# Kernel tuning notes

Hardware: AMD Instinct MI355X
Metric: run time of the kernel (lower is better)

The kernel has to match this reference:

```python
import jax, jax.numpy as jnp
import numpy as np


def setup_inputs() -> dict:
    key = jax.random.key(0)
    ks = jax.random.split(key, 10)
    b, n, d = 4, 64, 64
    E = 4096
    node_emb = jax.random.normal(ks[0], (b * n, d), dtype=jnp.float32)
    path_emb = jax.random.normal(ks[1], (b, n, n, d), dtype=jnp.float32)
    edge_index = jax.random.randint(ks[2], (2, E), 0, b * n, dtype=jnp.int64)
    # learned params, stored as (in, out) so application is x @ W + b
    W_hz = jax.random.normal(ks[3], (d, d), dtype=jnp.float32) / np.sqrt(d)
    b_hz = jnp.zeros((d,), dtype=jnp.float32)
    W_zz = jax.random.normal(ks[4], (3 * d, d), dtype=jnp.float32) / np.sqrt(3 * d)
    b_zz = jnp.zeros((d,), dtype=jnp.float32)
    W_nm = jax.random.normal(ks[5], (2 * d, d), dtype=jnp.float32) / np.sqrt(2 * d)
    b_nm = jnp.zeros((d,), dtype=jnp.float32)
    return {
        "node_emb": node_emb, "path_emb": path_emb, "edge_index": edge_index,
        "W_hz": W_hz, "b_hz": b_hz, "W_zz": W_zz, "b_zz": b_zz,
        "W_nm": W_nm, "b_nm": b_nm,
    }


def reference(node_emb, path_emb, edge_index, W_hz, b_hz, W_zz, b_zz, W_nm, b_nm):
    b, n, _, d = path_emb.shape
    # ---- PathConv (aggr='max') ----
    z = path_emb @ W_hz + b_hz                                  # (b, n, n, d)
    # tropical (max-plus) matmul over paths: z_conv[b,i,j,d] = max_k z[b,i,k,d] + z[b,k,j,d]
    z_conv = jnp.max(z[:, :, :, None, :] + z[:, None, :, :, :], axis=2)  # (b, n, n, d)
    z = jnp.maximum(z_conv, z)                                  # path_aggr mode='max'
    ne = node_emb.reshape(b, n, d)
    n_i = jnp.broadcast_to(ne[:, :, None, :], (b, n, n, d))
    n_j = jnp.broadcast_to(ne[:, None, :, :], (b, n, n, d))
    u_path = jax.nn.relu(jnp.concatenate([n_i, z, n_j], axis=-1) @ W_zz + b_zz)
    # ---- MPLayer (default message = x_j, aggr='add'; edge_attr unused) ----
    src, dst = edge_index[0], edge_index[1]
    aggr_msg = jax.ops.segment_sum(node_emb[src], dst, num_segments=node_emb.shape[0])
    u_node = jax.nn.relu(jnp.concatenate([node_emb, aggr_msg], axis=-1) @ W_nm + b_nm)
    # residual
    return (u_node + node_emb, u_path + path_emb)
```

## Files before the change

kernel.cpp:

```cpp
#include <hip/hip_runtime.h>


__global__ __launch_bounds__(1024) void k_pathlin_node(
    const float* __restrict__ ne, const float* __restrict__ pe,
    const int* __restrict__ eidx,
    const float* __restrict__ Whz, const float* __restrict__ bhz,
    const float* __restrict__ Wzz,
    const float* __restrict__ Wnm, const float* __restrict__ bnm,
    float* __restrict__ zt, float* __restrict__ a1, float* __restrict__ a3,
    float* __restrict__ out0) {
  int bi = blockIdx.x;
  int b = bi >> 6, i = bi & 63;
  int t = threadIdx.x, lane = t & 63, w = t >> 6;
  __shared__ float sP[4096];
  __shared__ float sW[4096];
  __shared__ float part[16][64];
  __shared__ float nl[64], al[64];
  ((float4*)sP)[t] = ((const float4*)(pe + (size_t)bi * 4096))[t];
  ((float4*)sW)[t] = ((const float4*)Whz)[t];
  float bv = bhz[lane];
  if (w == 0) nl[lane] = ne[bi * 64 + lane];
  __syncthreads();
  float acc[4] = {bv, bv, bv, bv};
  int k0 = w * 4;
#pragma unroll
  for (int c = 0; c < 64; c += 4) {
    float w0 = sW[(c + 0) * 64 + lane], w1 = sW[(c + 1) * 64 + lane];
    float w2 = sW[(c + 2) * 64 + lane], w3 = sW[(c + 3) * 64 + lane];
#pragma unroll
    for (int kk = 0; kk < 4; ++kk) {
      const float4 p = *(const float4*)&sP[(k0 + kk) * 64 + c];
      acc[kk] += p.x * w0 + p.y * w1 + p.z * w2 + p.w * w3;
    }
  }
  float* dst = zt + (size_t)b * 262144 + (size_t)lane * 4096 + (size_t)i * 64 + k0;
  *(float4*)dst = make_float4(acc[0], acc[1], acc[2], acc[3]);
  __syncthreads();
  int* elist = (int*)sP;
  const int* srcv = eidx;
  const int* dstv = eidx + 4096;
  int cntw = 0;
  unsigned long long ltmask = (lane == 63) ? 0x7fffffffffffffffull
                                           : ((1ull << lane) - 1ull);
#pragma unroll
  for (int q = 0; q < 4; ++q) {
    int e2 = w * 256 + q * 64 + lane;
    bool match = (dstv[e2] == bi);
    unsigned long long mask = __ballot(match);
    if (match) {
      int pos = cntw + __popcll(mask & ltmask);
      elist[w * 256 + pos] = srcv[e2];
    }
    cntw += __popcll(mask);
  }
  float accA = 0.f;
  for (int m = 0; m < cntw; ++m) accA += ne[elist[w * 256 + m] * 64 + lane];
  part[w][lane] = accA;
  __syncthreads();
  if (w == 0) {
    float s = 0.f;
#pragma unroll
    for (int p2 = 0; p2 < 16; ++p2) s += part[p2][lane];
    al[lane] = s;
  } else if (w == 2) {
    const float* nr = ne + bi * 64;
    float s1 = 0.f;
    for (int d2 = 0; d2 < 64; ++d2) s1 += nr[d2] * Wzz[d2 * 64 + lane];
    a1[bi * 64 + lane] = s1;
  } else if (w == 3) {
    const float* nr = ne + bi * 64;
    float s3 = 0.f;
    for (int d2 = 0; d2 < 64; ++d2) s3 += nr[d2] * Wzz[(128 + d2) * 64 + lane];
    a3[bi * 64 + lane] = s3;
  }
  __syncthreads();
  {
    float s = 0.f;
#pragma unroll
    for (int dd = 0; dd < 4; ++dd) {
      int d2 = w * 4 + dd;
      s += nl[d2] * Wnm[d2 * 64 + lane] + al[d2] * Wnm[(64 + d2) * 64 + lane];
    }
    part[w][lane] = s;
  }
  __syncthreads();
  if (w == 0) {
    float v = bnm[lane];
#pragma unroll
    for (int p2 = 0; p2 < 16; ++p2) v += part[p2][lane];
    v = fmaxf(v, 0.f);
    out0[bi * 64 + lane] = v + nl[lane];
  }
}

__global__ __launch_bounds__(1024) void k_tropical(
    const float* __restrict__ zt, float* __restrict__ zt2) {
  int slice = blockIdx.x;
  int t = threadIdx.x, lane = t & 63, w = t >> 6;
  __shared__ float A[4096];
  const float* Ag = zt + (size_t)slice * 4096;
  ((float4*)A)[t] = ((const float4*)Ag)[t];
  float colreg[64];
#pragma unroll
  for (int k = 0; k < 64; ++k) colreg[k] = Ag[k * 64 + lane];
  int i0 = w * 4;
  float acc[4];
#pragma unroll
  for (int ii = 0; ii < 4; ++ii) acc[ii] = Ag[(i0 + ii) * 64 + lane];
  __syncthreads();
#pragma unroll
  for (int k = 0; k < 64; k += 4) {
#pragma unroll
    for (int ii = 0; ii < 4; ++ii) {
      const float4 a = *(const float4*)&A[(i0 + ii) * 64 + k];
      float m0 = fmaxf(a.x + colreg[k], a.y + colreg[k + 1]);
      float m1 = fmaxf(a.z + colreg[k + 2], a.w + colreg[k + 3]);
      acc[ii] = fmaxf(acc[ii], fmaxf(m0, m1));
    }
  }
  float* Og = zt2 + (size_t)slice * 4096 + (size_t)i0 * 64;
#pragma unroll
  for (int ii = 0; ii < 4; ++ii) Og[ii * 64 + lane] = acc[ii];
}

__global__ __launch_bounds__(1024) void k_upath(
    const float* __restrict__ zt2, const float* __restrict__ Wzz,
    const float* __restrict__ bzz, const float* __restrict__ a1,
    const float* __restrict__ a3, const float* __restrict__ pe,
    float* __restrict__ out1) {
  int bi = blockIdx.x;
  int b = bi >> 6, i = bi & 63;
  int t = threadIdx.x, lane = t & 63, w = t >> 6;
  __shared__ float sZ[4096];
  {
    int d2 = t >> 4, jo = (t & 15) * 4;
    const float* src = zt2 + (size_t)b * 262144 + (size_t)d2 * 4096
                     + (size_t)i * 64 + jo;
    *(float4*)&sZ[d2 * 64 + jo] = *(const float4*)src;
  }
  float wreg[64];
#pragma unroll
  for (int d = 0; d < 64; ++d) wreg[d] = Wzz[(64 + d) * 64 + lane];
  float base = a1[bi * 64 + lane] + bzz[lane];
  __syncthreads();
  int j0 = w * 4;
  float acc[4] = {base, base, base, base};
#pragma unroll
  for (int d = 0; d < 64; ++d) {
    const float4 z4 = *(const float4*)&sZ[d * 64 + j0];
    float wv = wreg[d];
    acc[0] += z4.x * wv;
    acc[1] += z4.y * wv;
    acc[2] += z4.z * wv;
    acc[3] += z4.w * wv;
  }
  const float* a3b = a3 + (size_t)b * 4096;
  size_t ob = (size_t)bi * 4096 + (size_t)j0 * 64;
#pragma unroll
  for (int jj = 0; jj < 4; ++jj) {
    float v = acc[jj] + a3b[(j0 + jj) * 64 + lane];
    v = fmaxf(v, 0.f);
    out1[ob + jj * 64 + lane] = v + pe[ob + jj * 64 + lane];
  }
}

extern "C" void kernel_launch(void* const* d_in, const int* in_sizes, int n_in,
                              void* d_out, int out_size, void* d_ws, size_t ws_size,
                              hipStream_t stream) {
  const float* node = (const float*)d_in[0];
  const float* pe   = (const float*)d_in[1];
  const int*   eidx = (const int*)d_in[2];
  const float* Whz  = (const float*)d_in[3];
  const float* bhz  = (const float*)d_in[4];
  const float* Wzz  = (const float*)d_in[5];
  const float* bzz  = (const float*)d_in[6];
  const float* Wnm  = (const float*)d_in[7];
  const float* bnm  = (const float*)d_in[8];
  float* out0 = (float*)d_out;
  float* out1 = out0 + 16384;
  float* zt  = (float*)d_ws;
  float* zt2 = zt + 1048576;
  float* a1  = zt2 + 1048576;
  float* a3  = a1 + 16384;

  hipLaunchKernelGGL(k_pathlin_node, dim3(256), dim3(1024), 0, stream,
                     node, pe, eidx, Whz, bhz, Wzz, Wnm, bnm, zt, a1, a3, out0);
  hipLaunchKernelGGL(k_tropical, dim3(256), dim3(1024), 0, stream, zt, zt2);
  hipLaunchKernelGGL(k_upath, dim3(256), dim3(1024), 0, stream,
                     zt2, Wzz, bzz, a1, a3, pe, out1);
}
```

Baseline: 28.12 us.

## Fuse tropical max-plus product into the u_path projection kernel

```diff
diff --git a/kernel.cpp b/kernel.cpp
--- a/kernel.cpp
+++ b/kernel.cpp
@@ -93,61 +93,61 @@
   }
 }
 
-__global__ __launch_bounds__(1024) void k_tropical(
-    const float* __restrict__ zt, float* __restrict__ zt2) {
-  int slice = blockIdx.x;
-  int t = threadIdx.x, lane = t & 63, w = t >> 6;
-  __shared__ float A[4096];
-  const float* Ag = zt + (size_t)slice * 4096;
-  ((float4*)A)[t] = ((const float4*)Ag)[t];
-  float colreg[64];
-#pragma unroll
-  for (int k = 0; k < 64; ++k) colreg[k] = Ag[k * 64 + lane];
-  int i0 = w * 4;
-  float acc[4];
-#pragma unroll
-  for (int ii = 0; ii < 4; ++ii) acc[ii] = Ag[(i0 + ii) * 64 + lane];
-  __syncthreads();
-#pragma unroll
-  for (int k = 0; k < 64; k += 4) {
-#pragma unroll
-    for (int ii = 0; ii < 4; ++ii) {
-      const float4 a = *(const float4*)&A[(i0 + ii) * 64 + k];
-      float m0 = fmaxf(a.x + colreg[k], a.y + colreg[k + 1]);
-      float m1 = fmaxf(a.z + colreg[k + 2], a.w + colreg[k + 3]);
-      acc[ii] = fmaxf(acc[ii], fmaxf(m0, m1));
-    }
-  }
-  float* Og = zt2 + (size_t)slice * 4096 + (size_t)i0 * 64;
-#pragma unroll
-  for (int ii = 0; ii < 4; ++ii) Og[ii * 64 + lane] = acc[ii];
-}
-
-__global__ __launch_bounds__(1024) void k_upath(
-    const float* __restrict__ zt2, const float* __restrict__ Wzz,
+__global__ __launch_bounds__(1024) void k_tropupath(
+    const float* __restrict__ zt, const float* __restrict__ Wzz,
     const float* __restrict__ bzz, const float* __restrict__ a1,
     const float* __restrict__ a3, const float* __restrict__ pe,
     float* __restrict__ out1) {
   int bi = blockIdx.x;
   int b = bi >> 6, i = bi & 63;
   int t = threadIdx.x, lane = t & 63, w = t >> 6;
-  __shared__ float sZ[4096];
+  __shared__ float R[4096];
   {
-    int d2 = t >> 4, jo = (t & 15) * 4;
-    const float* src = zt2 + (size_t)b * 262144 + (size_t)d2 * 4096
-                     + (size_t)i * 64 + jo;
-    *(float4*)&sZ[d2 * 64 + jo] = *(const float4*)src;
+    int d = t >> 4, ko = (t & 15) * 4;
+    *(float4*)&R[d * 64 + ko] = *(const float4*)(
+        zt + (size_t)b * 262144 + (size_t)d * 4096 + (size_t)i * 64 + ko);
   }
   float wreg[64];
 #pragma unroll
   for (int d = 0; d < 64; ++d) wreg[d] = Wzz[(64 + d) * 64 + lane];
   float base = a1[bi * 64 + lane] + bzz[lane];
   __syncthreads();
+  {
+    int d0 = w * 4;
+    const float* A0 = zt + (size_t)b * 262144 + (size_t)(d0 + 0) * 4096;
+    const float* A1 = A0 + 4096;
+    const float* A2 = A1 + 4096;
+    const float* A3 = A2 + 4096;
+    float acc0 = R[(d0 + 0) * 64 + lane];
+    float acc1 = R[(d0 + 1) * 64 + lane];
+    float acc2 = R[(d0 + 2) * 64 + lane];
+    float acc3 = R[(d0 + 3) * 64 + lane];
+#pragma unroll 8
+    for (int k = 0; k < 64; ++k) {
+      float r0 = R[(d0 + 0) * 64 + k];
+      float r1 = R[(d0 + 1) * 64 + k];
+      float r2 = R[(d0 + 2) * 64 + k];
+      float r3 = R[(d0 + 3) * 64 + k];
+      float a0 = A0[k * 64 + lane];
+      float a1v = A1[k * 64 + lane];
+      float a2v = A2[k * 64 + lane];
+      float a3v = A3[k * 64 + lane];
+      acc0 = fmaxf(acc0, r0 + a0);
+      acc1 = fmaxf(acc1, r1 + a1v);
+      acc2 = fmaxf(acc2, r2 + a2v);
+      acc3 = fmaxf(acc3, r3 + a3v);
+    }
+    R[(d0 + 0) * 64 + lane] = acc0;
+    R[(d0 + 1) * 64 + lane] = acc1;
+    R[(d0 + 2) * 64 + lane] = acc2;
+    R[(d0 + 3) * 64 + lane] = acc3;
+  }
+  __syncthreads();
   int j0 = w * 4;
   float acc[4] = {base, base, base, base};
 #pragma unroll
   for (int d = 0; d < 64; ++d) {
-    const float4 z4 = *(const float4*)&sZ[d * 64 + j0];
+    const float4 z4 = *(const float4*)&R[d * 64 + j0];
     float wv = wreg[d];
     acc[0] += z4.x * wv;
     acc[1] += z4.y * wv;
@@ -179,13 +179,11 @@
   float* out0 = (float*)d_out;
   float* out1 = out0 + 16384;
   float* zt  = (float*)d_ws;
-  float* zt2 = zt + 1048576;
-  float* a1  = zt2 + 1048576;
+  float* a1  = zt + 1048576;
   float* a3  = a1 + 16384;
 
   hipLaunchKernelGGL(k_pathlin_node, dim3(256), dim3(1024), 0, stream,
                      node, pe, eidx, Whz, bhz, Wzz, Wnm, bnm, zt, a1, a3, out0);
-  hipLaunchKernelGGL(k_tropical, dim3(256), dim3(1024), 0, stream, zt, zt2);
-  hipLaunchKernelGGL(k_upath, dim3(256), dim3(1024), 0, stream,
-                     zt2, Wzz, bzz, a1, a3, pe, out1);
+  hipLaunchKernelGGL(k_tropupath, dim3(256), dim3(1024), 0, stream,
+                     zt, Wzz, bzz, a1, a3, pe, out1);
 }
```

Result: slower. 41.67 us (+48.2%).

## Split kernels into half-size blocks and move node update into tropical kernel

Applied to the files above, without the earlier changes.

```diff
diff --git a/kernel.cpp b/kernel.cpp
--- a/kernel.cpp
+++ b/kernel.cpp
@@ -1,153 +1,160 @@
 #include <hip/hip_runtime.h>
 
 
-__global__ __launch_bounds__(1024) void k_pathlin_node(
-    const float* __restrict__ ne, const float* __restrict__ pe,
-    const int* __restrict__ eidx,
-    const float* __restrict__ Whz, const float* __restrict__ bhz,
-    const float* __restrict__ Wzz,
-    const float* __restrict__ Wnm, const float* __restrict__ bnm,
-    float* __restrict__ zt, float* __restrict__ a1, float* __restrict__ a3,
-    float* __restrict__ out0) {
-  int bi = blockIdx.x;
+__global__ __launch_bounds__(512) void k_pathlin(
+    const float* __restrict__ pe, const float* __restrict__ Whz,
+    const float* __restrict__ bhz, float* __restrict__ zt) {
+  int blk = blockIdx.x;
+  int bi = blk >> 1, kh = blk & 1;
   int b = bi >> 6, i = bi & 63;
   int t = threadIdx.x, lane = t & 63, w = t >> 6;
-  __shared__ float sP[4096];
+  __shared__ float sP[2048];
   __shared__ float sW[4096];
-  __shared__ float part[16][64];
-  __shared__ float nl[64], al[64];
-  ((float4*)sP)[t] = ((const float4*)(pe + (size_t)bi * 4096))[t];
-  ((float4*)sW)[t] = ((const float4*)Whz)[t];
+  ((float4*)sP)[t] = ((const float4*)(pe + (size_t)bi * 4096 + kh * 2048))[t];
+  ((float4*)sW)[t]       = ((const float4*)Whz)[t];
+  ((float4*)sW)[t + 512] = ((const float4*)Whz)[t + 512];
   float bv = bhz[lane];
-  if (w == 0) nl[lane] = ne[bi * 64 + lane];
   __syncthreads();
   float acc[4] = {bv, bv, bv, bv};
-  int k0 = w * 4;
+  int kl = w * 4;
 #pragma unroll
   for (int c = 0; c < 64; c += 4) {
     float w0 = sW[(c + 0) * 64 + lane], w1 = sW[(c + 1) * 64 + lane];
     float w2 = sW[(c + 2) * 64 + lane], w3 = sW[(c + 3) * 64 + lane];
 #pragma unroll
     for (int kk = 0; kk < 4; ++kk) {
-      const float4 p = *(const float4*)&sP[(k0 + kk) * 64 + c];
+      const float4 p = *(const float4*)&sP[(kl + kk) * 64 + c];
       acc[kk] += p.x * w0 + p.y * w1 + p.z * w2 + p.w * w3;
     }
   }
+  int k0 = kh * 32 + kl;
   float* dst = zt + (size_t)b * 262144 + (size_t)lane * 4096 + (size_t)i * 64 + k0;
   *(float4*)dst = make_float4(acc[0], acc[1], acc[2], acc[3]);
-  __syncthreads();
-  int* elist = (int*)sP;
-  const int* srcv = eidx;
-  const int* dstv = eidx + 4096;
-  int cntw = 0;
-  unsigned long long ltmask = (lane == 63) ? 0x7fffffffffffffffull
-                                           : ((1ull << lane) - 1ull);
+}
+
+__global__ __launch_bounds__(512) void k_trop_node(
+    const float* __restrict__ zt, float* __restrict__ zt2,
+    const float* __restrict__ ne, const int* __restrict__ eidx,
+    const float* __restrict__ Wzz, const float* __restrict__ Wnm,
+    const float* __restrict__ bnm,
+    float* __restrict__ a1, float* __restrict__ a3, float* __restrict__ out0) {
+  int t = threadIdx.x, lane = t & 63, w = t >> 6;
+  __shared__ int elist[4096];
+  __shared__ float part[8][64];
+  __shared__ float nlal[2][64];
+  float* A = (float*)elist;
+  if (blockIdx.x < 512) {
+    int slice = blockIdx.x >> 1, ih = blockIdx.x & 1;
+    const float* Ag = zt + (size_t)slice * 4096;
+    ((float4*)A)[t] = ((const float4*)(Ag + ih * 2048))[t];
+    float colreg[64];
 #pragma unroll
-  for (int q = 0; q < 4; ++q) {
-    int e2 = w * 256 + q * 64 + lane;
-    bool match = (dstv[e2] == bi);
-    unsigned long long mask = __ballot(match);
-    if (match) {
-      int pos = cntw + __popcll(mask & ltmask);
-      elist[w * 256 + pos] = srcv[e2];
+    for (int k = 0; k < 64; ++k) colreg[k] = Ag[k * 64 + lane];
+    int il = w * 4, i0 = ih * 32 + il;
+    float acc[4];
+#pragma unroll
+    for (int ii = 0; ii < 4; ++ii) acc[ii] = Ag[(i0 + ii) * 64 + lane];
+    __syncthreads();
+#pragma unroll
+    for (int k = 0; k < 64; k += 4) {
+#pragma unroll
+      for (int ii = 0; ii < 4; ++ii) {
+        const float4 a = *(const float4*)&A[(il + ii) * 64 + k];
+        float m0 = fmaxf(a.x + colreg[k], a.y + colreg[k + 1]);
+        float m1 = fmaxf(a.z + colreg[k + 2], a.w + colreg[k + 3]);
+        acc[ii] = fmaxf(acc[ii], fmaxf(m0, m1));
+      }
     }
-    cntw += __popcll(mask);
-  }
-  float accA = 0.f;
-  for (int m = 0; m < cntw; ++m) accA += ne[elist[w * 256 + m] * 64 + lane];
-  part[w][lane] = accA;
-  __syncthreads();
-  if (w == 0) {
-    float s = 0.f;
+    float* Og = zt2 + (size_t)slice * 4096 + (size_t)i0 * 64;
 #pragma unroll
-    for (int p2 = 0; p2 < 16; ++p2) s += part[p2][lane];
-    al[lane] = s;
-  } else if (w == 2) {
-    const float* nr = ne + bi * 64;
-    float s1 = 0.f;
-    for (int d2 = 0; d2 < 64; ++d2) s1 += nr[d2] * Wzz[d2 * 64 + lane];
-    a1[bi * 64 + lane] = s1;
-  } else if (w == 3) {
-    const float* nr = ne + bi * 64;
-    float s3 = 0.f;
-    for (int d2 = 0; d2 < 64; ++d2) s3 += nr[d2] * Wzz[(128 + d2) * 64 + lane];
-    a3[bi * 64 + lane] = s3;
-  }
-  __syncthreads();
-  {
-    float s = 0.f;
+    for (int ii = 0; ii < 4; ++ii) Og[ii * 64 + lane] = acc[ii];
+  } else {
+    int r = blockIdx.x - 512;
+    const int* srcv = eidx;
+    const int* dstv = eidx + 4096;
+    int cntw = 0;
+    unsigned long long ltmask = (lane == 63) ? 0x7fffffffffffffffull
+                                             : ((1ull << lane) - 1ull);
 #pragma unroll
-    for (int dd = 0; dd < 4; ++dd) {
-      int d2 = w * 4 + dd;
-      s += nl[d2] * Wnm[d2 * 64 + lane] + al[d2] * Wnm[(64 + d2) * 64 + lane];
+    for (int q = 0; q < 8; ++q) {
+      int e2 = w * 512 + q * 64 + lane;
+      bool match = (dstv[e2] == r);
+      unsigned long long mask = __ballot(match);
+      if (match) {
+        int pos = cntw + __popcll(mask & ltmask);
+        elist[w * 512 + pos] = srcv[e2];
+      }
+      cntw += __popcll(mask);
     }
-    part[w][lane] = s;
-  }
-  __syncthreads();
-  if (w == 0) {
-    float v = bnm[lane];
+    float accA = 0.f;
+    for (int m = 0; m < cntw; ++m) accA += ne[elist[w * 512 + m] * 64 + lane];
+    part[w][lane] = accA;
+    if (w == 0) nlal[0][lane] = ne[r * 64 + lane];
+    __syncthreads();
+    if (w == 0) {
+      float s = 0.f;
 #pragma unroll
-    for (int p2 = 0; p2 < 16; ++p2) v += part[p2][lane];
-    v = fmaxf(v, 0.f);
-    out0[bi * 64 + lane] = v + nl[lane];
+      for (int p2 = 0; p2 < 8; ++p2) s += part[p2][lane];
+      nlal[1][lane] = s;
+    } else if (w == 2) {
+      const float* nr = ne + r * 64;
+      float s1 = 0.f;
+      for (int d2 = 0; d2 < 64; ++d2) s1 += nr[d2] * Wzz[d2 * 64 + lane];
+      a1[r * 64 + lane] = s1;
+    } else if (w == 3) {
+      const float* nr = ne + r * 64;
+      float s3 = 0.f;
+      for (int d2 = 0; d2 < 64; ++d2) s3 += nr[d2] * Wzz[(128 + d2) * 64 + lane];
+      a3[r * 64 + lane] = s3;
+    }
+    __syncthreads();
+    {
+      float s = 0.f;
+#pragma unroll
+      for (int dd = 0; dd < 8; ++dd) {
+        int d2 = w * 8 + dd;
+        s += nlal[0][d2] * Wnm[d2 * 64 + lane]
+           + nlal[1][d2] * Wnm[(64 + d2) * 64 + lane];
+      }
+      part[w][lane] = s;
+    }
+    __syncthreads();
+    if (w == 0) {
+      float v = bnm[lane];
+#pragma unroll
+      for (int p2 = 0; p2 < 8; ++p2) v += part[p2][lane];
+      v = fmaxf(v, 0.f);
+      out0[r * 64 + lane] = v + nlal[0][lane];
+    }
   }
 }
 
-__global__ __launch_bounds__(1024) void k_tropical(
-    const float* __restrict__ zt, float* __restrict__ zt2) {
-  int slice = blockIdx.x;
-  int t = threadIdx.x, lane = t & 63, w = t >> 6;
-  __shared__ float A[4096];
-  const float* Ag = zt + (size_t)slice * 4096;
-  ((float4*)A)[t] = ((const float4*)Ag)[t];
-  float colreg[64];
-#pragma unroll
-  for (int k = 0; k < 64; ++k) colreg[k] = Ag[k * 64 + lane];
-  int i0 = w * 4;
-  float acc[4];
-#pragma unroll
-  for (int ii = 0; ii < 4; ++ii) acc[ii] = Ag[(i0 + ii) * 64 + lane];
-  __syncthreads();
-#pragma unroll
-  for (int k = 0; k < 64; k += 4) {
-#pragma unroll
-    for (int ii = 0; ii < 4; ++ii) {
-      const float4 a = *(const float4*)&A[(i0 + ii) * 64 + k];
-      float m0 = fmaxf(a.x + colreg[k], a.y + colreg[k + 1]);
-      float m1 = fmaxf(a.z + colreg[k + 2], a.w + colreg[k + 3]);
-      acc[ii] = fmaxf(acc[ii], fmaxf(m0, m1));
-    }
-  }
-  float* Og = zt2 + (size_t)slice * 4096 + (size_t)i0 * 64;
-#pragma unroll
-  for (int ii = 0; ii < 4; ++ii) Og[ii * 64 + lane] = acc[ii];
-}
-
-__global__ __launch_bounds__(1024) void k_upath(
+__global__ __launch_bounds__(512) void k_upath(
     const float* __restrict__ zt2, const float* __restrict__ Wzz,
     const float* __restrict__ bzz, const float* __restrict__ a1,
     const float* __restrict__ a3, const float* __restrict__ pe,
     float* __restrict__ out1) {
-  int bi = blockIdx.x;
+  int blk = blockIdx.x;
+  int bi = blk >> 1, jh = blk & 1;
   int b = bi >> 6, i = bi & 63;
   int t = threadIdx.x, lane = t & 63, w = t >> 6;
-  __shared__ float sZ[4096];
+  __shared__ float sZ[2048];
   {
-    int d2 = t >> 4, jo = (t & 15) * 4;
+    int d2 = t >> 3, jo = (t & 7) * 4;
     const float* src = zt2 + (size_t)b * 262144 + (size_t)d2 * 4096
-                     + (size_t)i * 64 + jo;
-    *(float4*)&sZ[d2 * 64 + jo] = *(const float4*)src;
+                     + (size_t)i * 64 + jh * 32 + jo;
+    *(float4*)&sZ[d2 * 32 + jo] = *(const float4*)src;
   }
   float wreg[64];
 #pragma unroll
   for (int d = 0; d < 64; ++d) wreg[d] = Wzz[(64 + d) * 64 + lane];
   float base = a1[bi * 64 + lane] + bzz[lane];
   __syncthreads();
-  int j0 = w * 4;
+  int jl = w * 4, j0 = jh * 32 + jl;
   float acc[4] = {base, base, base, base};
 #pragma unroll
   for (int d = 0; d < 64; ++d) {
-    const float4 z4 = *(const float4*)&sZ[d * 64 + j0];
+    const float4 z4 = *(const float4*)&sZ[d * 32 + jl];
     float wv = wreg[d];
     acc[0] += z4.x * wv;
     acc[1] += z4.y * wv;
@@ -183,9 +190,9 @@
   float* a1  = zt2 + 1048576;
   float* a3  = a1 + 16384;
 
-  hipLaunchKernelGGL(k_pathlin_node, dim3(256), dim3(1024), 0, stream,
-                     node, pe, eidx, Whz, bhz, Wzz, Wnm, bnm, zt, a1, a3, out0);
-  hipLaunchKernelGGL(k_tropical, dim3(256), dim3(1024), 0, stream, zt, zt2);
-  hipLaunchKernelGGL(k_upath, dim3(256), dim3(1024), 0, stream,
+  hipLaunchKernelGGL(k_pathlin, dim3(512), dim3(512), 0, stream, pe, Whz, bhz, zt);
+  hipLaunchKernelGGL(k_trop_node, dim3(768), dim3(512), 0, stream,
+                     zt, zt2, node, eidx, Wzz, Wnm, bnm, a1, a3, out0);
+  hipLaunchKernelGGL(k_upath, dim3(512), dim3(512), 0, stream,
                      zt2, Wzz, bzz, a1, a3, pe, out1);
 }
```

Result: no change. 27.64 us (-1.7%).
